# Kernel optimization log

Hardware: AMD Instinct MI355X
Metric: run time of the kernel (lower is better)

The kernel has to match this reference:

```python
import jax, jax.numpy as jnp
import numpy as np

C = 19
IGNORE = 255
UPPER_BOUND = 1.0
SEG_W, EDGE_W, ATT_W = 1.0, 0.3, 0.1
EDGE_THRESH = 0.8


def _img_hist(t):
    # torch.histc(target, bins=C, min=0, max=C): bin i counts values in [i, i+1); 255 falls outside
    tf = t.ravel()
    inb = (tf >= 0) & (tf < C)
    idx = jnp.where(inb, tf, 0)
    return jnp.zeros((C,), jnp.float32).at[idx].add(inb.astype(jnp.float32))


def _seg_loss(segin, target):
    # per-image class-histogram weights (ImageBasedCrossEntropyLoss2d, norm=False)
    N = target.shape[0]
    bins = jax.vmap(_img_hist)(target)                      # [N, C]
    hist_norm = bins / jnp.sum(bins, axis=1, keepdims=True)
    w = (bins != 0).astype(jnp.float32) * UPPER_BOUND * (1.0 - hist_norm) + 1.0  # [N, C]

    logp = jax.nn.log_softmax(segin, axis=1)                # [N, C, H, W]
    tc = jnp.clip(target, 0, C - 1)
    lp = jnp.take_along_axis(logp, tc[:, None, :, :], axis=1)[:, 0]  # [N, H, W]
    valid = (target != IGNORE).astype(jnp.float32)
    pw = jnp.take_along_axis(w, tc.reshape(N, -1), axis=1).reshape(target.shape) * valid
    # NLLLoss(weight, reduction='mean', ignore_index): weighted mean per image, summed over batch
    num = -jnp.sum(pw * lp, axis=(1, 2))
    den = jnp.sum(pw, axis=(1, 2))
    return jnp.sum(num / den)


def _bce2d(x, t):
    # x: logits [N,1,H,W]; t: float target, 1=pos, 0=neg, >1 ignored (weight 0)
    pos = t == 1.0
    neg = t == 0.0
    pos_num = jnp.sum(pos.astype(jnp.float32))
    neg_num = jnp.sum(neg.astype(jnp.float32))
    sum_num = pos_num + neg_num
    w = jnp.where(pos, neg_num / sum_num, 0.0) + jnp.where(neg, pos_num / sum_num, 0.0)
    # stable BCE-with-logits
    bce = jnp.maximum(x, 0.0) - x * t + jnp.log1p(jnp.exp(-jnp.abs(x)))
    return jnp.mean(w * bce)


def setup_inputs() -> dict:
    key = jax.random.key(0)
    k1, k2, k3, k4 = jax.random.split(key, 4)
    N, H, W = 4, 768, 768
    segin = jax.random.normal(k1, (N, C, H, W), dtype=jnp.float32)
    edgein = jax.random.normal(k2, (N, 1, H, W), dtype=jnp.float32)
    segmask = jax.random.randint(k3, (N, H, W), 0, C, dtype=jnp.int32)
    edgemask = jax.random.randint(k4, (N, 1, H, W), 0, 2, dtype=jnp.int32)
    return {"segin": segin, "edgein": edgein, "segmask": segmask, "edgemask": edgemask}


def reference(segin, edgein, segmask, edgemask):
    seg_loss = SEG_W * _seg_loss(segin, segmask)
    edge_loss = EDGE_W * _bce2d(edgein, edgemask.astype(jnp.float32))
    # edge attention: pixels where max-channel edge logit > 0.8 keep their label, else ignore
    edge_max = jnp.max(edgein, axis=1)                      # [N, H, W]
    att_target = jnp.where(edge_max > EDGE_THRESH, segmask, IGNORE)
    att_loss = ATT_W * _seg_loss(segin, att_target)
    return seg_loss + edge_loss + att_loss
```

## Files before the change

kernel.cpp:

```cpp
#include <hip/hip_runtime.h>
#include <math.h>

#define CNUM 19
#define NB 4
#define HW 589824
#define NPIX 2359296

struct Ws {
  unsigned int hist_seg[NB][CNUM];
  unsigned int hist_att[NB][CNUM];
  unsigned int pos_num;
  unsigned int neg_num;
  double num_seg[NB];
  double den_seg[NB];
  double num_att[NB];
  double den_att[NB];
  double bce_sum;
};

__global__ void k_init(Ws* ws) {
  unsigned int* p = (unsigned int*)ws;
  const int nwords = (int)(sizeof(Ws) / 4);
  for (int i = threadIdx.x; i < nwords; i += blockDim.x) p[i] = 0u;
}

__global__ __launch_bounds__(256) void k_hist(const int* __restrict__ segmask,
                                              const float* __restrict__ edgein,
                                              const int* __restrict__ edgemask,
                                              Ws* __restrict__ ws) {
  const int n  = blockIdx.y;
  const int bx = blockIdx.x;
  const int tid = threadIdx.x;
  const int base = n * HW + bx * 4096 + tid * 4;

  unsigned int cs[CNUM], ca[CNUM];
  #pragma unroll
  for (int c = 0; c < CNUM; ++c) { cs[c] = 0u; ca[c] = 0u; }
  unsigned int cp = 0u, cn = 0u;

  #pragma unroll
  for (int it = 0; it < 4; ++it) {
    const int idx = base + it * 1024;
    int4   sv = *reinterpret_cast<const int4*>(segmask + idx);
    float4 e  = *reinterpret_cast<const float4*>(edgein + idx);
    int4   mv = *reinterpret_cast<const int4*>(edgemask + idx);
    int   sa[4] = {sv.x, sv.y, sv.z, sv.w};
    float ea[4] = {e.x, e.y, e.z, e.w};
    int   ma[4] = {mv.x, mv.y, mv.z, mv.w};
    #pragma unroll
    for (int p = 0; p < 4; ++p) {
      const int s = sa[p];
      const bool inb = ((unsigned)s) < (unsigned)CNUM;
      const unsigned long long attm = __ballot(ea[p] > 0.8f);
      #pragma unroll
      for (int c = 0; c < CNUM; ++c) {
        unsigned long long bm = __ballot(inb && (s == c));
        cs[c] += (unsigned)__popcll(bm);
        ca[c] += (unsigned)__popcll(bm & attm);
      }
      cp += (unsigned)__popcll(__ballot(ma[p] == 1));
      cn += (unsigned)__popcll(__ballot(ma[p] == 0));
    }
  }

  __shared__ unsigned int red[4][2 * CNUM + 2];
  const int wave = tid >> 6;
  const int lane = tid & 63;
  if (lane == 0) {
    #pragma unroll
    for (int c = 0; c < CNUM; ++c) { red[wave][c] = cs[c]; red[wave][CNUM + c] = ca[c]; }
    red[wave][2 * CNUM] = cp;
    red[wave][2 * CNUM + 1] = cn;
  }
  __syncthreads();
  if (tid < 2 * CNUM + 2) {
    unsigned int v = red[0][tid] + red[1][tid] + red[2][tid] + red[3][tid];
    if (tid < CNUM)               atomicAdd(&ws->hist_seg[n][tid], v);
    else if (tid < 2 * CNUM)      atomicAdd(&ws->hist_att[n][tid - CNUM], v);
    else if (tid == 2 * CNUM)     atomicAdd(&ws->pos_num, v);
    else                          atomicAdd(&ws->neg_num, v);
  }
}

__global__ __launch_bounds__(256, 4) void k_main(const float* __restrict__ segin,
                                                 const float* __restrict__ edgein,
                                                 const int* __restrict__ segmask,
                                                 const int* __restrict__ edgemask,
                                                 const Ws* __restrict__ ws,
                                                 Ws* __restrict__ wsw) {
  const int n = blockIdx.y;
  const int tid = threadIdx.x;
  const int hw4 = (blockIdx.x * 256 + tid) * 4;
  const int idx4 = n * HW + hw4;
  const float* base = segin + (size_t)n * CNUM * HW + hw4;

  __shared__ float lws[CNUM], lwa[CNUM];
  if (tid < CNUM) {
    float total = 0.f;
    #pragma unroll
    for (int i = 0; i < CNUM; ++i) total += (float)ws->hist_seg[n][i];
    float bins = (float)ws->hist_seg[n][tid];
    lws[tid] = (bins != 0.f ? (1.0f - bins / total) : 0.f) + 1.0f;
  } else if (tid >= 64 && tid < 64 + CNUM) {
    int c = tid - 64;
    float total = 0.f;
    #pragma unroll
    for (int i = 0; i < CNUM; ++i) total += (float)ws->hist_att[n][i];
    float bins = (float)ws->hist_att[n][c];
    lwa[c] = (bins != 0.f ? (1.0f - bins / total) : 0.f) + 1.0f;
  }

  float4 xv[CNUM];
  #pragma unroll
  for (int c = 0; c < CNUM; ++c)
    xv[c] = *reinterpret_cast<const float4*>(base + (size_t)c * HW);
  int4   tm = *reinterpret_cast<const int4*>(segmask + idx4);
  float4 ev = *reinterpret_cast<const float4*>(edgein + idx4);
  int4   em = *reinterpret_cast<const int4*>(edgemask + idx4);

  const unsigned int pn = ws->pos_num, nn = ws->neg_num;
  const float inv_sum = 1.0f / (float)(pn + nn);
  const float wpos = (float)nn * inv_sum;
  const float wneg = (float)pn * inv_sum;

  __syncthreads();

  int   tarr[4]  = {tm.x, tm.y, tm.z, tm.w};
  float earr[4]  = {ev.x, ev.y, ev.z, ev.w};
  int   emarr[4] = {em.x, em.y, em.z, em.w};

  float acc_num_s = 0.f, acc_den_s = 0.f, acc_num_a = 0.f, acc_den_a = 0.f, acc_bce = 0.f;
  #pragma unroll
  for (int p = 0; p < 4; ++p) {
    const int t = tarr[p];
    const int tc = min(max(t, 0), CNUM - 1);
    const float* xp = (const float*)&xv[0] + p;
    float s = 0.f, xt = 0.f;
    #pragma unroll
    for (int c = 0; c < CNUM; ++c) {
      float v = xp[4 * c];
      s += __expf(v);
      xt = (tc == c) ? v : xt;
    }
    float lp = xt - __logf(s);

    bool validt = (t != 255);
    float pw_s = validt ? lws[tc] : 0.f;
    acc_num_s -= pw_s * lp;
    acc_den_s += pw_s;

    float e = earr[p];
    bool valida = validt && (e > 0.8f);
    float pw_a = valida ? lwa[tc] : 0.f;
    acc_num_a -= pw_a * lp;
    acc_den_a += pw_a;

    int emv = emarr[p];
    float tf = (float)emv;
    float wb = (emv == 1) ? wpos : ((emv == 0) ? wneg : 0.f);
    float bce = fmaxf(e, 0.f) - e * tf + log1pf(__expf(-fabsf(e)));
    acc_bce += wb * bce;
  }

  #pragma unroll
  for (int off = 32; off > 0; off >>= 1) {
    acc_num_s += __shfl_down(acc_num_s, off);
    acc_den_s += __shfl_down(acc_den_s, off);
    acc_num_a += __shfl_down(acc_num_a, off);
    acc_den_a += __shfl_down(acc_den_a, off);
    acc_bce   += __shfl_down(acc_bce, off);
  }
  __shared__ float red[4][5];
  const int wave = tid >> 6;
  const int lane = tid & 63;
  if (lane == 0) {
    red[wave][0] = acc_num_s; red[wave][1] = acc_den_s;
    red[wave][2] = acc_num_a; red[wave][3] = acc_den_a;
    red[wave][4] = acc_bce;
  }
  __syncthreads();
  if (tid == 0) {
    float r0 = 0.f, r1 = 0.f, r2 = 0.f, r3 = 0.f, r4 = 0.f;
    #pragma unroll
    for (int wv = 0; wv < 4; ++wv) {
      r0 += red[wv][0]; r1 += red[wv][1]; r2 += red[wv][2];
      r3 += red[wv][3]; r4 += red[wv][4];
    }
    atomicAdd(&wsw->num_seg[n], (double)r0);
    atomicAdd(&wsw->den_seg[n], (double)r1);
    atomicAdd(&wsw->num_att[n], (double)r2);
    atomicAdd(&wsw->den_att[n], (double)r3);
    atomicAdd(&wsw->bce_sum,    (double)r4);
  }
}

__global__ void k_final(const Ws* __restrict__ ws, float* __restrict__ out) {
  if (threadIdx.x == 0 && blockIdx.x == 0) {
    double segl = 0.0, attl = 0.0;
    for (int i = 0; i < NB; ++i) {
      segl += ws->num_seg[i] / ws->den_seg[i];
      attl += ws->num_att[i] / ws->den_att[i];
    }
    double edgel = ws->bce_sum / (double)NPIX;
    out[0] = (float)(1.0 * segl + 0.3 * edgel + 0.1 * attl);
  }
}

extern "C" void kernel_launch(void* const* d_in, const int* in_sizes, int n_in,
                              void* d_out, int out_size, void* d_ws, size_t ws_size,
                              hipStream_t stream) {
  const float* segin   = (const float*)d_in[0];
  const float* edgein  = (const float*)d_in[1];
  const int*   segmask = (const int*)d_in[2];
  const int*   edgemask= (const int*)d_in[3];
  Ws* ws = (Ws*)d_ws;
  float* out = (float*)d_out;

  hipLaunchKernelGGL(k_init,  dim3(1),             dim3(256), 0, stream, ws);
  hipLaunchKernelGGL(k_hist,  dim3(HW / 4096, NB), dim3(256), 0, stream, segmask, edgein, edgemask, ws);
  hipLaunchKernelGGL(k_main,  dim3(HW / 1024, NB), dim3(256), 0, stream, segin, edgein, segmask, edgemask, ws, ws);
  hipLaunchKernelGGL(k_final, dim3(1),             dim3(1),   0, stream, ws, out);
}
```

Before: 345.8 us.

## Restructure main loss kernel to stream channels over 16 pixels per thread

The main kernel now gives each thread 16 pixels instead of 4, in 128-thread blocks. It loops over the 19 channels, loading four float4 per channel and keeping running exp-sums and target logits, rather than holding all 19 channel vectors in registers at once. Mask data is packed into bitfields to save registers, and the block-level reduction shrinks to two waves. The aim is more memory-level parallelism per thread and fewer, larger blocks with fewer atomics, at the cost of more live registers per thread and fewer total threads.

```diff
diff --git a/kernel.cpp b/kernel.cpp
--- a/kernel.cpp
+++ b/kernel.cpp
@@ -5,6 +5,9 @@
 #define NB 4
 #define HW 589824
 #define NPIX 2359296
+#define TPB 128
+#define PXT 16
+#define TILE (TPB * PXT)
 
 struct Ws {
   unsigned int hist_seg[NB][CNUM];
@@ -20,8 +23,8 @@
 
 __global__ void k_init(Ws* ws) {
   unsigned int* p = (unsigned int*)ws;
-  const int nwords = (int)(sizeof(Ws) / 4);
-  for (int i = threadIdx.x; i < nwords; i += blockDim.x) p[i] = 0u;
+  const int nw = (int)(sizeof(Ws) / 4);
+  for (int i = threadIdx.x; i < nw; i += blockDim.x) p[i] = 0u;
 }
 
 __global__ __launch_bounds__(256) void k_hist(const int* __restrict__ segmask,
@@ -82,84 +85,109 @@
   }
 }
 
-__global__ __launch_bounds__(256, 4) void k_main(const float* __restrict__ segin,
-                                                 const float* __restrict__ edgein,
-                                                 const int* __restrict__ segmask,
-                                                 const int* __restrict__ edgemask,
-                                                 const Ws* __restrict__ ws,
-                                                 Ws* __restrict__ wsw) {
+__global__ __launch_bounds__(TPB) void k_main(const float* __restrict__ segin,
+                                              const float* __restrict__ edgein,
+                                              const int* __restrict__ segmask,
+                                              const int* __restrict__ edgemask,
+                                              const Ws* __restrict__ ws,
+                                              Ws* __restrict__ wsw) {
   const int n = blockIdx.y;
-  const int tid = threadIdx.x;
-  const int hw4 = (blockIdx.x * 256 + tid) * 4;
-  const int idx4 = n * HW + hw4;
-  const float* base = segin + (size_t)n * CNUM * HW + hw4;
+  const int t = threadIdx.x;
+  const int tile0 = blockIdx.x * TILE;
 
   __shared__ float lws[CNUM], lwa[CNUM];
-  if (tid < CNUM) {
+  __shared__ float redlds[2][5];
+
+  if (t < CNUM) {
     float total = 0.f;
     #pragma unroll
     for (int i = 0; i < CNUM; ++i) total += (float)ws->hist_seg[n][i];
-    float bins = (float)ws->hist_seg[n][tid];
-    lws[tid] = (bins != 0.f ? (1.0f - bins / total) : 0.f) + 1.0f;
-  } else if (tid >= 64 && tid < 64 + CNUM) {
-    int c = tid - 64;
+    float bins = (float)ws->hist_seg[n][t];
+    lws[t] = (bins != 0.f ? (1.0f - bins / total) : 0.f) + 1.0f;
+  } else if (t >= 64 && t < 64 + CNUM) {
+    int c = t - 64;
     float total = 0.f;
     #pragma unroll
     for (int i = 0; i < CNUM; ++i) total += (float)ws->hist_att[n][i];
     float bins = (float)ws->hist_att[n][c];
     lwa[c] = (bins != 0.f ? (1.0f - bins / total) : 0.f) + 1.0f;
   }
-
-  float4 xv[CNUM];
-  #pragma unroll
-  for (int c = 0; c < CNUM; ++c)
-    xv[c] = *reinterpret_cast<const float4*>(base + (size_t)c * HW);
-  int4   tm = *reinterpret_cast<const int4*>(segmask + idx4);
-  float4 ev = *reinterpret_cast<const float4*>(edgein + idx4);
-  int4   em = *reinterpret_cast<const int4*>(edgemask + idx4);
-
   const unsigned int pn = ws->pos_num, nn = ws->neg_num;
   const float inv_sum = 1.0f / (float)(pn + nn);
   const float wpos = (float)nn * inv_sum;
   const float wneg = (float)pn * inv_sum;
-
   __syncthreads();
 
-  int   tarr[4]  = {tm.x, tm.y, tm.z, tm.w};
-  float earr[4]  = {ev.x, ev.y, ev.z, ev.w};
-  int   emarr[4] = {em.x, em.y, em.z, em.w};
+  const int pxbase = n * HW + tile0;
+
+  int tcv[PXT];
+  unsigned int validbits = 0u;
+  unsigned int embits = 0u;
+  float4 ev[4];
+  #pragma unroll
+  for (int k = 0; k < 4; ++k) {
+    const int off = pxbase + (k * TPB + t) * 4;
+    int4 tm = *reinterpret_cast<const int4*>(segmask + off);
+    ev[k]   = *reinterpret_cast<const float4*>(edgein + off);
+    int4 em = *reinterpret_cast<const int4*>(edgemask + off);
+    int ta[4] = {tm.x, tm.y, tm.z, tm.w};
+    int ea[4] = {em.x, em.y, em.z, em.w};
+    #pragma unroll
+    for (int j = 0; j < 4; ++j) {
+      const int p = k * 4 + j;
+      tcv[p] = min(max(ta[j], 0), CNUM - 1);
+      validbits |= (ta[j] != 255) ? (1u << p) : 0u;
+      embits |= ((unsigned)(ea[j] & 3)) << (2 * p);
+    }
+  }
+
+  float sacc[PXT], xt[PXT];
+  #pragma unroll
+  for (int p = 0; p < PXT; ++p) { sacc[p] = 0.f; xt[p] = 0.f; }
+
+  const float* cb = segin + (size_t)n * CNUM * HW + tile0;
+  #pragma unroll
+  for (int c = 0; c < CNUM; ++c) {
+    float4 v[4];
+    #pragma unroll
+    for (int k = 0; k < 4; ++k)
+      v[k] = *reinterpret_cast<const float4*>(cb + (size_t)c * HW + (k * TPB + t) * 4);
+    #pragma unroll
+    for (int k = 0; k < 4; ++k) {
+      float va[4] = {v[k].x, v[k].y, v[k].z, v[k].w};
+      #pragma unroll
+      for (int j = 0; j < 4; ++j) {
+        const int p = k * 4 + j;
+        sacc[p] += __expf(va[j]);
+        xt[p] = (tcv[p] == c) ? va[j] : xt[p];
+      }
+    }
+  }
 
   float acc_num_s = 0.f, acc_den_s = 0.f, acc_num_a = 0.f, acc_den_a = 0.f, acc_bce = 0.f;
   #pragma unroll
-  for (int p = 0; p < 4; ++p) {
-    const int t = tarr[p];
-    const int tc = min(max(t, 0), CNUM - 1);
-    const float* xp = (const float*)&xv[0] + p;
-    float s = 0.f, xt = 0.f;
-    #pragma unroll
-    for (int c = 0; c < CNUM; ++c) {
-      float v = xp[4 * c];
-      s += __expf(v);
-      xt = (tc == c) ? v : xt;
-    }
-    float lp = xt - __logf(s);
-
-    bool validt = (t != 255);
-    float pw_s = validt ? lws[tc] : 0.f;
-    acc_num_s -= pw_s * lp;
-    acc_den_s += pw_s;
-
-    float e = earr[p];
-    bool valida = validt && (e > 0.8f);
-    float pw_a = valida ? lwa[tc] : 0.f;
-    acc_num_a -= pw_a * lp;
-    acc_den_a += pw_a;
-
-    int emv = emarr[p];
-    float tf = (float)emv;
-    float wb = (emv == 1) ? wpos : ((emv == 0) ? wneg : 0.f);
-    float bce = fmaxf(e, 0.f) - e * tf + log1pf(__expf(-fabsf(e)));
-    acc_bce += wb * bce;
+  for (int k = 0; k < 4; ++k) {
+    float ea[4] = {ev[k].x, ev[k].y, ev[k].z, ev[k].w};
+    #pragma unroll
+    for (int j = 0; j < 4; ++j) {
+      const int p = k * 4 + j;
+      float lp = xt[p] - __logf(sacc[p]);
+      bool valid = (validbits >> p) & 1u;
+      float pw_s = valid ? lws[tcv[p]] : 0.f;
+      acc_num_s -= pw_s * lp;
+      acc_den_s += pw_s;
+
+      float e = ea[j];
+      bool valida = valid && (e > 0.8f);
+      float pw_a = valida ? lwa[tcv[p]] : 0.f;
+      acc_num_a -= pw_a * lp;
+      acc_den_a += pw_a;
+
+      int emv = (int)((embits >> (2 * p)) & 3u);
+      float bce = fmaxf(e, 0.f) - e * (float)emv + log1pf(__expf(-fabsf(e)));
+      float wb = (emv == 1) ? wpos : ((emv == 0) ? wneg : 0.f);
+      acc_bce += wb * bce;
+    }
   }
 
   #pragma unroll
@@ -170,22 +198,20 @@
     acc_den_a += __shfl_down(acc_den_a, off);
     acc_bce   += __shfl_down(acc_bce, off);
   }
-  __shared__ float red[4][5];
-  const int wave = tid >> 6;
-  const int lane = tid & 63;
+  const int wave = t >> 6;
+  const int lane = t & 63;
   if (lane == 0) {
-    red[wave][0] = acc_num_s; red[wave][1] = acc_den_s;
-    red[wave][2] = acc_num_a; red[wave][3] = acc_den_a;
-    red[wave][4] = acc_bce;
+    redlds[wave][0] = acc_num_s; redlds[wave][1] = acc_den_s;
+    redlds[wave][2] = acc_num_a; redlds[wave][3] = acc_den_a;
+    redlds[wave][4] = acc_bce;
   }
   __syncthreads();
-  if (tid == 0) {
-    float r0 = 0.f, r1 = 0.f, r2 = 0.f, r3 = 0.f, r4 = 0.f;
-    #pragma unroll
-    for (int wv = 0; wv < 4; ++wv) {
-      r0 += red[wv][0]; r1 += red[wv][1]; r2 += red[wv][2];
-      r3 += red[wv][3]; r4 += red[wv][4];
-    }
+  if (t == 0) {
+    float r0 = redlds[0][0] + redlds[1][0];
+    float r1 = redlds[0][1] + redlds[1][1];
+    float r2 = redlds[0][2] + redlds[1][2];
+    float r3 = redlds[0][3] + redlds[1][3];
+    float r4 = redlds[0][4] + redlds[1][4];
     atomicAdd(&wsw->num_seg[n], (double)r0);
     atomicAdd(&wsw->den_seg[n], (double)r1);
     atomicAdd(&wsw->num_att[n], (double)r2);
@@ -202,7 +228,7 @@
       attl += ws->num_att[i] / ws->den_att[i];
     }
     double edgel = ws->bce_sum / (double)NPIX;
-    out[0] = (float)(1.0 * segl + 0.3 * edgel + 0.1 * attl);
+    out[0] = (float)(segl + 0.3 * edgel + 0.1 * attl);
   }
 }
 
@@ -216,8 +242,8 @@
   Ws* ws = (Ws*)d_ws;
   float* out = (float*)d_out;
 
-  hipLaunchKernelGGL(k_init,  dim3(1),             dim3(256), 0, stream, ws);
-  hipLaunchKernelGGL(k_hist,  dim3(HW / 4096, NB), dim3(256), 0, stream, segmask, edgein, edgemask, ws);
-  hipLaunchKernelGGL(k_main,  dim3(HW / 1024, NB), dim3(256), 0, stream, segin, edgein, segmask, edgemask, ws, ws);
-  hipLaunchKernelGGL(k_final, dim3(1),             dim3(1),   0, stream, ws, out);
-}
+  hipLaunchKernelGGL(k_init,  dim3(1),              dim3(128), 0, stream, ws);
+  hipLaunchKernelGGL(k_hist,  dim3(HW / 4096, NB),  dim3(256), 0, stream, segmask, edgein, edgemask, ws);
+  hipLaunchKernelGGL(k_main,  dim3(HW / TILE, NB),  dim3(TPB), 0, stream, segin, edgein, segmask, edgemask, ws, ws);
+  hipLaunchKernelGGL(k_final, dim3(1),              dim3(1),   0, stream, ws, out);
+}
```

Measured after the change: 322.5 us. 1.07x faster.
